# Kernel tuning notes

Hardware: AMD Instinct MI355X
Metric: run time of the kernel (lower is better)

Reference implementation:

```python
import jax, jax.numpy as jnp
from jax import lax
import numpy as np

B, IN, OUT = 32768, 512, 512


def _bit_length(a):
    # a: nonnegative int32. Smear high bit down, then popcount == bit length.
    y = a
    y = y | (y >> 1)
    y = y | (y >> 2)
    y = y | (y >> 4)
    y = y | (y >> 8)
    y = y | (y >> 16)
    return lax.population_count(y)


def trunc_top_bits(v, k=4):
    # compress_top4(|a|,|b|,4): keep top-k significant bits of each magnitude.
    a = jnp.abs(v)
    shift = jnp.maximum(_bit_length(a) - k, 0)
    t = (a >> shift) << shift
    return t * jnp.sign(v)


def setup_inputs() -> dict:
    key = jax.random.key(0)
    k1, k2, k3 = jax.random.split(key, 3)
    bound = 1.0 / np.sqrt(IN)  # matches kaiming_uniform(a=sqrt(5)) + bias bound
    x = jax.random.normal(k1, (B, IN), dtype=jnp.float32)
    weight = jax.random.uniform(k2, (OUT, IN), dtype=jnp.float32, minval=-bound, maxval=bound)
    bias = jax.random.uniform(k3, (OUT,), dtype=jnp.float32, minval=-bound, maxval=bound)
    return {"x": x, "weight": weight, "bias": bias, "weight_sf": 8, "act_sf": 6}


def reference(x, weight, bias, weight_sf, act_sf):
    # Fixed-point quantization: input / 2^{-sf} then trunc-toward-zero int cast
    xi = (x * (2.0 ** act_sf)).astype(jnp.int32)       # [B, IN]
    wi = (weight * (2.0 ** weight_sf)).astype(jnp.int32)  # [OUT, IN]
    # sign/abs decomposition + top-4-bit truncated multiply-accumulate:
    # sum_y compress_top4(|xi|,|wi|) * sign(xi)*sign(wi) == dot of signed truncs
    tx = trunc_top_bits(xi).astype(jnp.float32)
    tw = trunc_top_bits(wi).astype(jnp.float32)
    acc = jnp.einsum("bi,oi->bo", tx, tw)             # [B, OUT], exact in fp32
    scale = (2.0 ** (-act_sf)) * (2.0 ** (-weight_sf))
    return acc * scale + bias[None, :]
```

## Files before the change

### kernel.cpp

```cpp
#include <hip/hip_runtime.h>
#include <stdint.h>

#define B_DIM 32768
#define IN_DIM 512
#define OUT_DIM 512

typedef float f32x4 __attribute__((ext_vector_type(4)));
typedef long long2_t __attribute__((ext_vector_type(2)));

__device__ __forceinline__ float trunc4(float x, float s) {
    uint32_t u = __float_as_uint(truncf(x * s));
    return __uint_as_float(u & 0xFFF00000u);
}

__global__ void quant_fp8_2(const float* __restrict__ x, const float* __restrict__ w,
                            uint32_t* __restrict__ ox, uint32_t* __restrict__ ow,
                            int nx4, int nw4,
                            const int* __restrict__ asf, const int* __restrict__ wsf) {
    int i = blockIdx.x * blockDim.x + threadIdx.x;
    const float4* in;
    uint32_t* out;
    float scale;
    if (i < nx4) {
        in = (const float4*)x + i;  out = ox + i;  scale = (float)(1 << *asf);
    } else {
        int j = i - nx4;
        if (j >= nw4) return;
        in = (const float4*)w + j;  out = ow + j;  scale = (float)(1 << *wsf);
    }
    float4 v = *in;
    int p = 0;
    p = __builtin_amdgcn_cvt_pk_fp8_f32(trunc4(v.x, scale), trunc4(v.y, scale), p, false);
    p = __builtin_amdgcn_cvt_pk_fp8_f32(trunc4(v.z, scale), trunc4(v.w, scale), p, true);
    *out = (uint32_t)p;
}

__global__ __launch_bounds__(512, 4)
void gemm_f8(const uint8_t* __restrict__ A, const uint8_t* __restrict__ W,
             const float* __restrict__ bias, float* __restrict__ C,
             const int* __restrict__ wsf, const int* __restrict__ asf) {
    __shared__ uint8_t As[2][128 * 64];
    __shared__ uint8_t Bs[2][256 * 64];

    const int t    = threadIdx.x;
    const int w    = t >> 6;
    const int lane = t & 63;

    const int b    = blockIdx.x;
    const int xcd  = b & 7;
    const int bm   = xcd * 32 + (b >> 4);
    const int bn   = (b >> 3) & 1;
    const int row0 = bm * 128;
    const int col0 = bn * 256;
    const int wm   = (w & 1) * 64;
    const int wn   = (w >> 1) * 64;

    const int m_st = t >> 2;
    const int goff = ((2 * (t & 3)) ^ (m_st & 6)) * 8;
    const size_t offA = (size_t)(row0 + m_st) * IN_DIM + goff;
    const size_t offB = (size_t)(col0 + m_st) * IN_DIM + goff;

    f32x4 acc[4][4];
    #pragma unroll
    for (int mt = 0; mt < 4; ++mt)
        #pragma unroll
        for (int nt = 0; nt < 4; ++nt)
            acc[mt][nt] = 0.0f;

    {
        const uint8_t* ga = A + offA;
        uint8_t*       la = &As[0][w * 1024];
        __builtin_amdgcn_global_load_lds((const __attribute__((address_space(1))) void*)ga,
                                         (__attribute__((address_space(3))) void*)la, 16, 0, 0);
        #pragma unroll
        for (int i = 0; i < 2; ++i) {
            const uint8_t* gb = W + offB + (size_t)i * 128 * IN_DIM;
            uint8_t*       lb = &Bs[0][i * 8192 + w * 1024];
            __builtin_amdgcn_global_load_lds((const __attribute__((address_space(1))) void*)gb,
                                             (__attribute__((address_space(3))) void*)lb, 16, 0, 0);
        }
    }
    asm volatile("s_waitcnt vmcnt(0) lgkmcnt(0)" ::: "memory");
    __builtin_amdgcn_sched_barrier(0);
    __builtin_amdgcn_s_barrier();
    __builtin_amdgcn_sched_barrier(0);

    #pragma unroll
    for (int k = 0; k < 8; ++k) {
        const int cur = k & 1;
        const int nxt = cur ^ 1;

        if (k < 7) {
            const uint8_t* ga = A + offA + (k + 1) * 64;
            uint8_t*       la = &As[nxt][w * 1024];
            __builtin_amdgcn_global_load_lds((const __attribute__((address_space(1))) void*)ga,
                                             (__attribute__((address_space(3))) void*)la, 16, 0, 0);
            #pragma unroll
            for (int i = 0; i < 2; ++i) {
                const uint8_t* gb = W + offB + (size_t)i * 128 * IN_DIM + (k + 1) * 64;
                uint8_t*       lb = &Bs[nxt][i * 8192 + w * 1024];
                __builtin_amdgcn_global_load_lds((const __attribute__((address_space(1))) void*)gb,
                                                 (__attribute__((address_space(3))) void*)lb, 16, 0, 0);
            }
        }
        __builtin_amdgcn_sched_barrier(0);

        {
            const int q  = lane >> 4;
            const int rl = lane & 15;
            const int ch = (q ^ ((rl >> 1) & 3)) * 16;
            long2_t af[4], bfr[4];
            #pragma unroll
            for (int mt = 0; mt < 4; ++mt)
                af[mt] = *(const long2_t*)(&As[cur][0] + (wm + mt * 16 + rl) * 64 + ch);
            #pragma unroll
            for (int nt = 0; nt < 4; ++nt)
                bfr[nt] = *(const long2_t*)(&Bs[cur][0] + (wn + nt * 16 + rl) * 64 + ch);
            #pragma unroll
            for (int mt = 0; mt < 4; ++mt)
                #pragma unroll
                for (int nt = 0; nt < 4; ++nt) {
                    acc[mt][nt] = __builtin_amdgcn_mfma_f32_16x16x32_fp8_fp8(af[mt].x, bfr[nt].x, acc[mt][nt], 0, 0, 0);
                    acc[mt][nt] = __builtin_amdgcn_mfma_f32_16x16x32_fp8_fp8(af[mt].y, bfr[nt].y, acc[mt][nt], 0, 0, 0);
                }
        }

        if (k < 7) {
            asm volatile("s_waitcnt vmcnt(0) lgkmcnt(0)" ::: "memory");
            __builtin_amdgcn_sched_barrier(0);
            __builtin_amdgcn_s_barrier();
            __builtin_amdgcn_sched_barrier(0);
        }
    }

    const float oscale = ldexpf(1.0f, -(*wsf + *asf));
    const int cl = lane & 15;
    const int rg = (lane >> 4) * 4;
    #pragma unroll
    for (int nt = 0; nt < 4; ++nt) {
        const int col = col0 + wn + nt * 16 + cl;
        const float bv = bias[col];
        #pragma unroll
        for (int mt = 0; mt < 4; ++mt) {
            f32x4 a = acc[mt][nt];
            #pragma unroll
            for (int r = 0; r < 4; ++r) {
                const int row = row0 + wm + mt * 16 + rg + r;
                C[(size_t)row * OUT_DIM + col] = a[r] * oscale + bv;
            }
        }
    }
}

extern "C" void kernel_launch(void* const* d_in, const int* in_sizes, int n_in,
                              void* d_out, int out_size, void* d_ws, size_t ws_size,
                              hipStream_t stream) {
    const float* x    = (const float*)d_in[0];
    const float* wgt  = (const float*)d_in[1];
    const float* bias = (const float*)d_in[2];
    const int*   wsf  = (const int*)d_in[3];
    const int*   asf  = (const int*)d_in[4];

    uint8_t* tx = (uint8_t*)d_ws;
    uint8_t* tw = (uint8_t*)d_ws + (size_t)B_DIM * IN_DIM;

    const int nx4 = B_DIM * IN_DIM / 4;
    const int nw4 = OUT_DIM * IN_DIM / 4;
    quant_fp8_2<<<(nx4 + nw4 + 255) / 256, 256, 0, stream>>>(
        x, wgt, (uint32_t*)tx, (uint32_t*)tw, nx4, nw4, asf, wsf);

    const int grid = (B_DIM / 128) * (OUT_DIM / 256);
    gemm_f8<<<grid, 512, 0, stream>>>(tx, tw, bias, (float*)d_out, wsf, asf);
}
```

Measured before the change: 134.8 us.

## Fuse activation fp8 quantization into GEMM A-tile loading

Removes the separate pass that quantized x to fp8 in workspace. The GEMM now loads fp32 x tiles into registers, truncates and converts them to fp8, and writes them to swizzled LDS. Weight tiles move to a triple-buffered async-LDS pipeline. This avoids the fp8 intermediate write and re-read, but each x tile is read in fp32 by both column blocks and adds conversion ALU work inside the main loop.

```diff
diff --git a/kernel.cpp b/kernel.cpp
--- a/kernel.cpp
+++ b/kernel.cpp
@@ -13,52 +13,43 @@
     return __uint_as_float(u & 0xFFF00000u);
 }
 
-__global__ void quant_fp8_2(const float* __restrict__ x, const float* __restrict__ w,
-                            uint32_t* __restrict__ ox, uint32_t* __restrict__ ow,
-                            int nx4, int nw4,
-                            const int* __restrict__ asf, const int* __restrict__ wsf) {
+__global__ void quant_fp8(const float* __restrict__ in, uint32_t* __restrict__ out,
+                          int n4, const int* __restrict__ sf) {
     int i = blockIdx.x * blockDim.x + threadIdx.x;
-    const float4* in;
-    uint32_t* out;
-    float scale;
-    if (i < nx4) {
-        in = (const float4*)x + i;  out = ox + i;  scale = (float)(1 << *asf);
-    } else {
-        int j = i - nx4;
-        if (j >= nw4) return;
-        in = (const float4*)w + j;  out = ow + j;  scale = (float)(1 << *wsf);
-    }
-    float4 v = *in;
+    if (i >= n4) return;
+    float scale = (float)(1 << *sf);
+    float4 v = ((const float4*)in)[i];
     int p = 0;
     p = __builtin_amdgcn_cvt_pk_fp8_f32(trunc4(v.x, scale), trunc4(v.y, scale), p, false);
     p = __builtin_amdgcn_cvt_pk_fp8_f32(trunc4(v.z, scale), trunc4(v.w, scale), p, true);
-    *out = (uint32_t)p;
+    out[i] = (uint32_t)p;
 }
 
 __global__ __launch_bounds__(512, 4)
-void gemm_f8(const uint8_t* __restrict__ A, const uint8_t* __restrict__ W,
-             const float* __restrict__ bias, float* __restrict__ C,
-             const int* __restrict__ wsf, const int* __restrict__ asf) {
+void gemm_f8x(const float* __restrict__ X, const uint8_t* __restrict__ W,
+              const float* __restrict__ bias, float* __restrict__ C,
+              const int* __restrict__ wsf, const int* __restrict__ asf) {
     __shared__ uint8_t As[2][128 * 64];
-    __shared__ uint8_t Bs[2][256 * 64];
+    __shared__ uint8_t Ws[3][256 * 64];
 
     const int t    = threadIdx.x;
     const int w    = t >> 6;
     const int lane = t & 63;
 
     const int b    = blockIdx.x;
-    const int xcd  = b & 7;
-    const int bm   = xcd * 32 + (b >> 4);
+    const int bm   = (b & 7) * 32 + (b >> 4);
     const int bn   = (b >> 3) & 1;
     const int row0 = bm * 128;
     const int col0 = bn * 256;
     const int wm   = (w & 1) * 64;
     const int wn   = (w >> 1) * 64;
 
-    const int m_st = t >> 2;
-    const int goff = ((2 * (t & 3)) ^ (m_st & 6)) * 8;
-    const size_t offA = (size_t)(row0 + m_st) * IN_DIM + goff;
-    const size_t offB = (size_t)(col0 + m_st) * IN_DIM + goff;
+    const int mw   = t >> 2;
+    const size_t offW = (size_t)(col0 + mw) * IN_DIM + ((2 * (t & 3)) ^ (mw & 6)) * 8;
+
+    const float* xa = X + (size_t)(row0 + (t >> 3)) * IN_DIM + (t & 7) * 8;
+    const int awoff = ((t >> 3) * 8 + ((t & 7) ^ ((t >> 3) & 6))) * 8;
+    const float ascale = (float)(1 << *asf);
 
     f32x4 acc[4][4];
     #pragma unroll
@@ -67,42 +58,57 @@
         for (int nt = 0; nt < 4; ++nt)
             acc[mt][nt] = 0.0f;
 
-    {
-        const uint8_t* ga = A + offA;
-        uint8_t*       la = &As[0][w * 1024];
-        __builtin_amdgcn_global_load_lds((const __attribute__((address_space(1))) void*)ga,
-                                         (__attribute__((address_space(3))) void*)la, 16, 0, 0);
-        #pragma unroll
-        for (int i = 0; i < 2; ++i) {
-            const uint8_t* gb = W + offB + (size_t)i * 128 * IN_DIM;
-            uint8_t*       lb = &Bs[0][i * 8192 + w * 1024];
-            __builtin_amdgcn_global_load_lds((const __attribute__((address_space(1))) void*)gb,
-                                             (__attribute__((address_space(3))) void*)lb, 16, 0, 0);
-        }
+    float4 fr[2][2];
+
+#define ISSUE_W(s, kt)                                                                        \
+    {                                                                                         \
+        _Pragma("unroll")                                                                     \
+        for (int i = 0; i < 2; ++i) {                                                         \
+            const uint8_t* gw = W + offW + (size_t)i * 128 * IN_DIM + (kt) * 64;              \
+            uint8_t*       lw = &Ws[s][i * 8192 + w * 1024];                                  \
+            __builtin_amdgcn_global_load_lds((const __attribute__((address_space(1))) void*)gw,\
+                                             (__attribute__((address_space(3))) void*)lw, 16, 0, 0); \
+        }                                                                                     \
     }
-    asm volatile("s_waitcnt vmcnt(0) lgkmcnt(0)" ::: "memory");
+
+#define ISSUE_A(kt)                                                                           \
+    {                                                                                         \
+        _Pragma("unroll")                                                                     \
+        for (int g = 0; g < 2; ++g)                                                           \
+            _Pragma("unroll")                                                                 \
+            for (int h = 0; h < 2; ++h)                                                       \
+                fr[g][h] = *(const float4*)(xa + (size_t)g * 64 * IN_DIM + (kt) * 64 + h * 4);\
+    }
+
+#define QUANT_WRITE_A(s)                                                                      \
+    {                                                                                         \
+        _Pragma("unroll")                                                                     \
+        for (int g = 0; g < 2; ++g) {                                                         \
+            int p0 = 0, p1 = 0;                                                               \
+            p0 = __builtin_amdgcn_cvt_pk_fp8_f32(trunc4(fr[g][0].x, ascale), trunc4(fr[g][0].y, ascale), p0, false); \
+            p0 = __builtin_amdgcn_cvt_pk_fp8_f32(trunc4(fr[g][0].z, ascale), trunc4(fr[g][0].w, ascale), p0, true);  \
+            p1 = __builtin_amdgcn_cvt_pk_fp8_f32(trunc4(fr[g][1].x, ascale), trunc4(fr[g][1].y, ascale), p1, false); \
+            p1 = __builtin_amdgcn_cvt_pk_fp8_f32(trunc4(fr[g][1].z, ascale), trunc4(fr[g][1].w, ascale), p1, true);  \
+            uint2 pq; pq.x = (uint32_t)p0; pq.y = (uint32_t)p1;                               \
+            *(uint2*)(&As[s][awoff + g * 4096]) = pq;                                         \
+        }                                                                                     \
+    }
+
+    ISSUE_W(0, 0);
+    ISSUE_A(0);
+    ISSUE_W(1, 1);
+    asm volatile("s_waitcnt vmcnt(2)" ::: "memory");
+    __builtin_amdgcn_sched_barrier(0);
+    QUANT_WRITE_A(0);
+    asm volatile("s_waitcnt lgkmcnt(0)" ::: "memory");
     __builtin_amdgcn_sched_barrier(0);
     __builtin_amdgcn_s_barrier();
     __builtin_amdgcn_sched_barrier(0);
 
     #pragma unroll
     for (int k = 0; k < 8; ++k) {
-        const int cur = k & 1;
-        const int nxt = cur ^ 1;
-
-        if (k < 7) {
-            const uint8_t* ga = A + offA + (k + 1) * 64;
-            uint8_t*       la = &As[nxt][w * 1024];
-            __builtin_amdgcn_global_load_lds((const __attribute__((address_space(1))) void*)ga,
-                                             (__attribute__((address_space(3))) void*)la, 16, 0, 0);
-            #pragma unroll
-            for (int i = 0; i < 2; ++i) {
-                const uint8_t* gb = W + offB + (size_t)i * 128 * IN_DIM + (k + 1) * 64;
-                uint8_t*       lb = &Bs[nxt][i * 8192 + w * 1024];
-                __builtin_amdgcn_global_load_lds((const __attribute__((address_space(1))) void*)gb,
-                                                 (__attribute__((address_space(3))) void*)lb, 16, 0, 0);
-            }
-        }
+        if (k < 7) ISSUE_A(k + 1);
+        if (k < 6) ISSUE_W((k + 2) % 3, k + 2);
         __builtin_amdgcn_sched_barrier(0);
 
         {
@@ -112,10 +118,10 @@
             long2_t af[4], bfr[4];
             #pragma unroll
             for (int mt = 0; mt < 4; ++mt)
-                af[mt] = *(const long2_t*)(&As[cur][0] + (wm + mt * 16 + rl) * 64 + ch);
+                af[mt] = *(const long2_t*)(&As[k & 1][0] + (wm + mt * 16 + rl) * 64 + ch);
             #pragma unroll
             for (int nt = 0; nt < 4; ++nt)
-                bfr[nt] = *(const long2_t*)(&Bs[cur][0] + (wn + nt * 16 + rl) * 64 + ch);
+                bfr[nt] = *(const long2_t*)(&Ws[k % 3][0] + (wn + nt * 16 + rl) * 64 + ch);
             #pragma unroll
             for (int mt = 0; mt < 4; ++mt)
                 #pragma unroll
@@ -126,7 +132,14 @@
         }
 
         if (k < 7) {
-            asm volatile("s_waitcnt vmcnt(0) lgkmcnt(0)" ::: "memory");
+            if (k < 6) {
+                asm volatile("s_waitcnt vmcnt(2)" ::: "memory");
+            } else {
+                asm volatile("s_waitcnt vmcnt(0)" ::: "memory");
+            }
+            __builtin_amdgcn_sched_barrier(0);
+            QUANT_WRITE_A((k + 1) & 1);
+            asm volatile("s_waitcnt lgkmcnt(0)" ::: "memory");
             __builtin_amdgcn_sched_barrier(0);
             __builtin_amdgcn_s_barrier();
             __builtin_amdgcn_sched_barrier(0);
@@ -150,6 +163,9 @@
             }
         }
     }
+#undef ISSUE_W
+#undef ISSUE_A
+#undef QUANT_WRITE_A
 }
 
 extern "C" void kernel_launch(void* const* d_in, const int* in_sizes, int n_in,
@@ -161,14 +177,11 @@
     const int*   wsf  = (const int*)d_in[3];
     const int*   asf  = (const int*)d_in[4];
 
-    uint8_t* tx = (uint8_t*)d_ws;
-    uint8_t* tw = (uint8_t*)d_ws + (size_t)B_DIM * IN_DIM;
+    uint8_t* tw = (uint8_t*)d_ws;
 
-    const int nx4 = B_DIM * IN_DIM / 4;
     const int nw4 = OUT_DIM * IN_DIM / 4;
-    quant_fp8_2<<<(nx4 + nw4 + 255) / 256, 256, 0, stream>>>(
-        x, wgt, (uint32_t*)tx, (uint32_t*)tw, nx4, nw4, asf, wsf);
+    quant_fp8<<<(nw4 + 255) / 256, 256, 0, stream>>>(wgt, (uint32_t*)tw, nw4, wsf);
 
     const int grid = (B_DIM / 128) * (OUT_DIM / 256);
-    gemm_f8<<<grid, 512, 0, stream>>>(tx, tw, bias, (float*)d_out, wsf, asf);
+    gemm_f8x<<<grid, 512, 0, stream>>>(x, tw, bias, (float*)d_out, wsf, asf);
 }
```

Result: slower. 144.5 us (+7.2%).
